# Performance work log

Hardware: AMD Instinct MI355X
Metric: run time of the kernel (lower is better)

Reference implementation:

```python
import jax, jax.numpy as jnp
import numpy as np

B, S, H = 8, 1024, 768
NUM_HEADS, DH = 12, 64
A, T = 12, 64

def setup_inputs() -> dict:
    key = jax.random.key(0)
    ks = jax.random.split(key, 12)
    all_tokens = jax.random.normal(ks[0], (B, S, H), dtype=jnp.float32)
    aspect_tokens = jax.random.normal(ks[1], (B, A, H), dtype=jnp.float32)
    # ragged target slices: start in [0, S-17), length in [1, 16]
    starts = jax.random.randint(ks[2], (T,), 0, S - 17)
    lens = jax.random.randint(ks[3], (T,), 1, 17)
    target_pos_info = jnp.stack([starts, starts + lens], axis=-1).astype(jnp.int32)  # (T,2)
    target_batch_info = jnp.sort(jax.random.randint(ks[4], (T,), 0, B)).astype(jnp.int32)
    attention_mask = jnp.ones((B, S), dtype=jnp.int32)
    s = 0.02
    W1 = jax.random.normal(ks[5], (H, H), dtype=jnp.float32) * s
    b1 = jnp.zeros((H,), dtype=jnp.float32)
    Wq = jax.random.normal(ks[6], (H, NUM_HEADS, DH), dtype=jnp.float32) * s
    bq = jnp.zeros((NUM_HEADS, DH), dtype=jnp.float32)
    Wk = jax.random.normal(ks[7], (H, NUM_HEADS, DH), dtype=jnp.float32) * s
    bk = jnp.zeros((NUM_HEADS, DH), dtype=jnp.float32)
    Wc = jax.random.normal(ks[8], (2 * H, 1), dtype=jnp.float32) * s
    bc = jnp.zeros((1,), dtype=jnp.float32)
    return {"all_tokens": all_tokens, "aspect_tokens": aspect_tokens,
            "target_pos_info": target_pos_info, "target_batch_info": target_batch_info,
            "attention_mask": attention_mask,
            "W1": W1, "b1": b1, "Wq": Wq, "bq": bq, "Wk": Wk, "bk": bk,
            "Wc": Wc, "bc": bc}


def reference(all_tokens, aspect_tokens, target_pos_info, target_batch_info,
              attention_mask, W1, b1, Wq, bq, Wk, bk, Wc, bc):
    # linear_transform (shared for tokens and aspects), dropout = identity at eval
    h = jax.nn.relu(jnp.einsum('bsh,hg->bsg', all_tokens, W1) + b1)     # (B,S,H)
    # SelfAttention: q/k EinsumDense projections; value = raw key_states reshaped
    q = jnp.einsum('bsh,hkd->bskd', h, Wq) + bq                          # (B,S,K,D)
    k = jnp.einsum('bsh,hkd->bskd', h, Wk) + bk
    v = h.reshape(k.shape)                                               # faithful: reshape, no proj
    q = q * jax.lax.rsqrt(jnp.asarray(DH, q.dtype))
    scores = jnp.einsum('bskd,bqkd->bkqs', k, q)                         # (B,K,Q,S)
    mask_val = attention_mask[:, 0].astype(scores.dtype)                 # original uses mask[:, 0:1]
    scores = scores + ((1.0 - mask_val) * -10000.0)[:, None, None, None]
    probs = jax.nn.softmax(scores, axis=-1)
    out = jnp.einsum('bkqs,bskd->bqkd', probs, v).reshape(h.shape)       # (B,S,H)
    # ragged per-target slice mean: masked mean over positions [s0, s1)
    pos = jnp.arange(S)
    s0, s1 = target_pos_info[:, 0], target_pos_info[:, 1]
    span = ((pos[None, :] >= s0[:, None]) & (pos[None, :] < s1[:, None])).astype(out.dtype)  # (T,S)
    gathered = out[target_batch_info]                                    # (T,S,H)
    counts = jnp.maximum(span.sum(-1, keepdims=True), 1.0)
    rep = jnp.einsum('ts,tsh->th', span, gathered) / counts              # (T,H)
    # aspect hidden states and target-aspect pairing (batch-ordered concat)
    h_a = jax.nn.relu(jnp.einsum('bah,hg->bag', aspect_tokens, W1) + b1)  # (B,A,H)
    pair = jnp.concatenate([jnp.broadcast_to(rep[:, None, :], (rep.shape[0], A, H)),
                            h_a[target_batch_info]], axis=-1)             # (T,A,2H)
    t_a_logit = jnp.einsum('tac,co->tao', pair, Wc) + bc                  # (T,A,1)
    return t_a_logit
```

## Files before the change

kernel.cpp:

```cpp
#include <hip/hip_runtime.h>


typedef __attribute__((ext_vector_type(8))) short s8v;
typedef __attribute__((ext_vector_type(4))) short s4v;
typedef __attribute__((ext_vector_type(4))) float f4v;

#define AS1 __attribute__((address_space(1)))
#define AS3 __attribute__((address_space(3)))

__device__ __forceinline__ unsigned short f2bf(float f) {
  union { float f; unsigned u; } v; v.f = f;
  unsigned r = v.u + 0x7FFFu + ((v.u >> 16) & 1u);
  return (unsigned short)(r >> 16);
}

__device__ __forceinline__ float bf2f(unsigned short u) {
  union { unsigned u; float f; } v; v.u = ((unsigned)u) << 16;
  return v.f;
}

__device__ __forceinline__ void gl2lds16(const void* g, void* l) {
  __builtin_amdgcn_global_load_lds((const AS1 void*)g, (AS3 void*)l, 16, 0, 0);
}

__global__ __launch_bounds__(256) void k_prep(const float* __restrict__ asp,
                                              const float* __restrict__ W1,
                                              const float* __restrict__ Wq,
                                              const float* __restrict__ Wk,
                                              unsigned short* __restrict__ Abf,
                                              unsigned short* __restrict__ W1t,
                                              unsigned short* __restrict__ Wqt,
                                              unsigned short* __restrict__ Wkt,
                                              float* __restrict__ outz) {
  __shared__ float T[64][68];
  int bid = blockIdx.x;
  int tid = threadIdx.x;
  if (bid < 36) {
    int i = bid * 256 + tid;
    const float4* src = (const float4*)(asp + (size_t)i * 8);
    float4 a = src[0], b = src[1];
    s8v o;
    o[0] = (short)f2bf(a.x); o[1] = (short)f2bf(a.y);
    o[2] = (short)f2bf(a.z); o[3] = (short)f2bf(a.w);
    o[4] = (short)f2bf(b.x); o[5] = (short)f2bf(b.y);
    o[6] = (short)f2bf(b.z); o[7] = (short)f2bf(b.w);
    *(s8v*)(Abf + (size_t)i * 8) = o;
  } else if (bid < 468) {
    int wb = bid - 36;
    const float* W = (wb < 144) ? W1 : (wb < 288) ? Wq : Wk;
    unsigned short* Wt = (wb < 144) ? W1t : (wb < 288) ? Wqt : Wkt;
    int tile = wb % 144;
    int tr = (tile / 12) * 64;
    int tc = (tile % 12) * 64;
#pragma unroll
    for (int p = 0; p < 4; ++p) {
      int r = p * 16 + (tid >> 4);
      int c = (tid & 15) * 4;
      float4 v = *(const float4*)(W + (size_t)(tr + r) * 768 + tc + c);
      T[r][c] = v.x; T[r][c + 1] = v.y; T[r][c + 2] = v.z; T[r][c + 3] = v.w;
    }
    __syncthreads();
#pragma unroll
    for (int p = 0; p < 2; ++p) {
      int n = p * 32 + (tid >> 3);
      int k8 = (tid & 7) * 8;
      s8v o;
#pragma unroll
      for (int j = 0; j < 8; ++j) o[j] = (short)f2bf(T[k8 + j][n]);
      *(s8v*)(Wt + (size_t)(tc + n) * 768 + tr + k8) = o;
    }
  } else {
#pragma unroll
    for (int q = 0; q < 3; ++q) outz[tid + q * 256] = 0.f;
  }
}

template <int MODE, bool AF32>
__device__ __forceinline__ void gemm_tile(int m0, int n0,
    const unsigned short* __restrict__ A, const float* __restrict__ Af,
    const unsigned short* __restrict__ Bt,
    const float* __restrict__ bias, unsigned short* __restrict__ C,
    unsigned short* __restrict__ C2, const int* __restrict__ pos,
    const int* __restrict__ tbi, unsigned short* As, unsigned short* Bs,
    int* srcRow) {
  const int K = 768;
  int tid = threadIdx.x, lane = tid & 63, w = tid >> 6;

  if (MODE == 2) {
    if (tid < 128) {
      int r = m0 + tid;
      int t = r >> 4, j = r & 15;
      int s0 = pos[2 * t], s1 = pos[2 * t + 1];
      int s = s0 + j; if (s > s1 - 1) s = s1 - 1;
      srcRow[tid] = tbi[t] * 1024 + s;
    }
    __syncthreads();
  }

  int rsub = lane >> 3;
  int cXor = ((lane & 7) ^ rsub) * 8;
  const unsigned short* aSrc[4];
  const float* aSrcF[4];
  const unsigned short* bSrc[4];
#pragma unroll
  for (int i = 0; i < 4; ++i) {
    int lr = (w * 4 + i) * 8 + rsub;
    size_t grow;
    if (MODE == 2) grow = (size_t)srcRow[lr];
    else if (MODE == 3) { int rr = m0 + lr; grow = (size_t)(rr < 96 ? rr : 95); }
    else grow = (size_t)(m0 + lr);
    if (AF32) aSrcF[i] = Af + grow * K + cXor;
    else aSrc[i] = A + grow * K + cXor;
    bSrc[i] = Bt + (size_t)(n0 + lr) * K + cXor;
  }

  f4v acc[4][4];
#pragma unroll
  for (int i = 0; i < 4; ++i)
#pragma unroll
    for (int j = 0; j < 4; ++j) acc[i][j] = (f4v)(0.0f);

  int wm = (w >> 1) * 64, wn = (w & 1) * 64;
  int lc = lane & 15, lg = lane >> 4;
  int aIdx[4][2], bIdx[4][2];
#pragma unroll
  for (int mi = 0; mi < 4; ++mi) {
    int ra = wm + mi * 16 + lc;
    int rb = wn + mi * 16 + lc;
#pragma unroll
    for (int kk = 0; kk < 2; ++kk) {
      aIdx[mi][kk] = ra * 64 + (((kk * 4 + lg) ^ (ra & 7)) * 8);
      bIdx[mi][kk] = rb * 64 + (((kk * 4 + lg) ^ (rb & 7)) * 8);
    }
  }

  for (int k0 = 0; k0 < K; k0 += 64) {
#pragma unroll
    for (int i = 0; i < 4; ++i) gl2lds16(bSrc[i] + k0, Bs + (w * 4 + i) * 512);
    if (AF32) {
#pragma unroll
      for (int i = 0; i < 4; ++i) {
        const float* p = aSrcF[i] + k0;
        float4 v0 = *(const float4*)p;
        float4 v1 = *(const float4*)(p + 4);
        s8v o;
        o[0] = (short)f2bf(v0.x); o[1] = (short)f2bf(v0.y);
        o[2] = (short)f2bf(v0.z); o[3] = (short)f2bf(v0.w);
        o[4] = (short)f2bf(v1.x); o[5] = (short)f2bf(v1.y);
        o[6] = (short)f2bf(v1.z); o[7] = (short)f2bf(v1.w);
        *(s8v*)(As + (w * 4 + i) * 512 + lane * 8) = o;
      }
    } else {
#pragma unroll
      for (int i = 0; i < 4; ++i) gl2lds16(aSrc[i] + k0, As + (w * 4 + i) * 512);
    }
    __syncthreads();
#pragma unroll
    for (int kk = 0; kk < 2; ++kk) {
      s8v ar[4], br[4];
#pragma unroll
      for (int mi = 0; mi < 4; ++mi) ar[mi] = *(const s8v*)(As + aIdx[mi][kk]);
#pragma unroll
      for (int ni = 0; ni < 4; ++ni) br[ni] = *(const s8v*)(Bs + bIdx[ni][kk]);
#pragma unroll
      for (int mi = 0; mi < 4; ++mi)
#pragma unroll
        for (int ni = 0; ni < 4; ++ni)
          acc[mi][ni] = __builtin_amdgcn_mfma_f32_16x16x32_bf16(ar[mi], br[ni], acc[mi][ni], 0, 0, 0);
    }
    __syncthreads();
  }

  if (MODE == 0 || MODE == 1) {
    unsigned short* L = As;
#pragma unroll
    for (int mi = 0; mi < 4; ++mi) {
#pragma unroll
      for (int ni = 0; ni < 4; ++ni) {
        int coll = wn + ni * 16 + lc;
        float bv = bias[n0 + coll];
        int row0l = wm + mi * 16 + lg * 4;
        s4v pk;
#pragma unroll
        for (int r = 0; r < 4; ++r) {
          float x = acc[mi][ni][r] + bv;
          if (MODE == 0) x = x > 0.f ? x : 0.f;
          unsigned short hv = f2bf(x);
          pk[r] = (short)hv;
          int rowl = row0l + r;
          L[rowl * 128 + (((coll >> 3) ^ (rowl & 7)) * 8) + (coll & 7)] = hv;
        }
        if (MODE == 0) {
          int grow0 = m0 + row0l;
          int b = grow0 >> 10, s = grow0 & 1023;
          int gcol = n0 + coll;
          int kh = gcol >> 6, d = gcol & 63;
          *(s4v*)(C2 + ((size_t)((b * 12 + kh) * 64 + d)) * 1024 + s) = pk;
        }
      }
    }
    __syncthreads();
#pragma unroll
    for (int p = 0; p < 8; ++p) {
      int rowl = p * 16 + (tid >> 4);
      int cs = (tid & 15) * 8;
      int chunk = (cs >> 3) ^ (rowl & 7);
      s8v v = *(const s8v*)(L + rowl * 128 + chunk * 8);
      if (MODE == 0) {
        *(s8v*)(C + (size_t)(m0 + rowl) * 768 + n0 + cs) = v;
      } else {
        int gr = m0 + rowl;
        int b = gr >> 10, s = gr & 1023;
        int gcol = n0 + cs;
        int kh = gcol >> 6, d = gcol & 63;
        *(s8v*)(C + ((size_t)((b * 12 + kh) * 1024 + s)) * 64 + d) = v;
      }
    }
  } else {
#pragma unroll
    for (int mi = 0; mi < 4; ++mi) {
#pragma unroll
      for (int ni = 0; ni < 4; ++ni) {
        int col = n0 + wn + ni * 16 + lc;
        float bv = bias[col];
        int row0 = m0 + wm + mi * 16 + lg * 4;
#pragma unroll
        for (int r = 0; r < 4; ++r) {
          int row = row0 + r;
          float x = acc[mi][ni][r] + bv;
          if (MODE == 2) {
            x *= 0.125f;
            int t = row >> 4, j = row & 15;
            int kh = col >> 6, d = col & 63;
            C[(size_t)((t * 12 + kh) * 16 + j) * 64 + d] = f2bf(x);
          } else {
            x = x > 0.f ? x : 0.f;
            if (row < 96) C[(size_t)row * 768 + col] = f2bf(x);
          }
        }
      }
    }
  }
}

__global__ __launch_bounds__(256) void k_gemmA(const float* __restrict__ X,
                                               const float* __restrict__ asp,
                                               const unsigned short* __restrict__ W1t,
                                               const float* __restrict__ b1,
                                               unsigned short* __restrict__ Hbf,
                                               unsigned short* __restrict__ Vt,
                                               unsigned short* __restrict__ Ha) {
  __shared__ unsigned short LDSB[16384];
  __shared__ int srcRow[128];
  unsigned short* As = LDSB;
  unsigned short* Bs = LDSB + 8192;
  int bid = blockIdx.x;
  if (bid < 384) {
    bid = (bid & 7) * 48 + (bid >> 3);
    gemm_tile<0, true>((bid / 6) * 128, (bid % 6) * 128, (const unsigned short*)nullptr,
                       X, W1t, b1, Hbf, Vt, (const int*)nullptr, (const int*)nullptr,
                       As, Bs, srcRow);
  } else {
    int b2 = bid - 384;
    gemm_tile<3, true>(0, b2 * 128, (const unsigned short*)nullptr,
                       asp, W1t, b1, Ha, (unsigned short*)nullptr,
                       (const int*)nullptr, (const int*)nullptr, As, Bs, srcRow);
  }
}

__global__ __launch_bounds__(256) void k_gemmB(const unsigned short* __restrict__ Hbf,
                                               const unsigned short* __restrict__ Wkt,
                                               const float* __restrict__ bk,
                                               unsigned short* __restrict__ Khm,
                                               const unsigned short* __restrict__ Wqt,
                                               const float* __restrict__ bq,
                                               unsigned short* __restrict__ Qhm,
                                               const int* __restrict__ pos,
                                               const int* __restrict__ tbi) {
  __shared__ unsigned short LDSB[16384];
  __shared__ int srcRow[128];
  unsigned short* As = LDSB;
  unsigned short* Bs = LDSB + 8192;
  int bid = blockIdx.x;
  bid = (bid & 7) * 54 + (bid >> 3);
  if (bid < 384) {
    gemm_tile<1, false>((bid / 6) * 128, (bid % 6) * 128, Hbf, (const float*)nullptr,
                        Wkt, bk, Khm, (unsigned short*)nullptr,
                        (const int*)nullptr, (const int*)nullptr, As, Bs, srcRow);
  } else {
    int b2 = bid - 384;
    gemm_tile<2, false>((b2 / 6) * 128, (b2 % 6) * 128, Hbf, (const float*)nullptr,
                        Wqt, bq, Qhm, (unsigned short*)nullptr, pos, tbi,
                        As, Bs, srcRow);
  }
}

__global__ __launch_bounds__(256) void k_attn(const unsigned short* __restrict__ q_hm,
                                              const unsigned short* __restrict__ k_hm,
                                              const unsigned short* __restrict__ vt,
                                              const unsigned short* __restrict__ ha,
                                              const int* __restrict__ pos,
                                              const int* __restrict__ tbi,
                                              const float* __restrict__ Wc,
                                              const float* __restrict__ bc,
                                              float* __restrict__ outp) {
  __shared__ unsigned short P[16 * 1032];
  __shared__ float O[4][16][64];
  __shared__ float rsbuf[4][16];
  __shared__ float inv_rs[16];
  __shared__ float hpart[4];
  __shared__ float rabuf;

  int bid = blockIdx.x;
  bid = (bid & 7) * 96 + (bid >> 3);
  int t = bid / 12, kh = bid % 12;
  int b = tbi[t];
  int s0 = pos[2 * t], s1 = pos[2 * t + 1];
  int len = s1 - s0;
  int tid = threadIdx.x, lane = tid & 63, w = tid >> 6;
  int lg = lane >> 4, lc = lane & 15;

  const unsigned short* qb = q_hm + (size_t)((t * 12 + kh) * 16) * 64;
  s8v a0 = *(const s8v*)(qb + (size_t)lc * 64 + lg * 8);
  s8v a1 = *(const s8v*)(qb + (size_t)lc * 64 + 32 + lg * 8);

  const unsigned short* kb = k_hm + (size_t)((b * 12 + kh) * 1024) * 64;
  float rs[4] = {0.f, 0.f, 0.f, 0.f};
  for (int it = 0; it < 16; ++it) {
    int sb = it * 64 + w * 16;
    s8v b0 = *(const s8v*)(kb + (size_t)(sb + lc) * 64 + lg * 8);
    s8v b1 = *(const s8v*)(kb + (size_t)(sb + lc) * 64 + 32 + lg * 8);
    f4v c = (f4v)(0.0f);
    c = __builtin_amdgcn_mfma_f32_16x16x32_bf16(a0, b0, c, 0, 0, 0);
    c = __builtin_amdgcn_mfma_f32_16x16x32_bf16(a1, b1, c, 0, 0, 0);
#pragma unroll
    for (int r = 0; r < 4; ++r) {
      float p = __expf(c[r]);
      rs[r] += p;
      P[(lg * 4 + r) * 1032 + sb + lc] = f2bf(p);
    }
  }
#pragma unroll
  for (int m = 1; m < 16; m <<= 1) {
#pragma unroll
    for (int r = 0; r < 4; ++r) rs[r] += __shfl_xor(rs[r], m, 64);
  }
  if (lc == 0) {
#pragma unroll
    for (int r = 0; r < 4; ++r) rsbuf[w][lg * 4 + r] = rs[r];
  }
  __syncthreads();
  if (tid < 16)
    inv_rs[tid] = 1.0f / (rsbuf[0][tid] + rsbuf[1][tid] + rsbuf[2][tid] + rsbuf[3][tid]);

  const unsigned short* vb = vt + (size_t)((b * 12 + kh) * 64) * 1024;
  f4v oc[4];
#pragma unroll
  for (int n = 0; n < 4; ++n) oc[n] = (f4v)(0.0f);
  for (int it = 0; it < 8; ++it) {
    int s32 = it * 128 + w * 32;
    s8v pa = *(const s8v*)(P + lc * 1032 + s32 + lg * 8);
#pragma unroll
    for (int n = 0; n < 4; ++n) {
      s8v vbf = *(const s8v*)(vb + (size_t)(n * 16 + lc) * 1024 + s32 + lg * 8);
      oc[n] = __builtin_amdgcn_mfma_f32_16x16x32_bf16(pa, vbf, oc[n], 0, 0, 0);
    }
  }
#pragma unroll
  for (int n = 0; n < 4; ++n)
#pragma unroll
    for (int r = 0; r < 4; ++r) O[w][lg * 4 + r][n * 16 + lc] = oc[n][r];
  __syncthreads();
  if (w == 0) {
    float sum = 0.f;
    for (int j = 0; j < len; ++j) {
      float v = O[0][j][lane] + O[1][j][lane] + O[2][j][lane] + O[3][j][lane];
      sum += v * inv_rs[j];
    }
    float repd = sum / (float)len;
    float pr = repd * Wc[kh * 64 + lane];
#pragma unroll
    for (int m = 1; m < 64; m <<= 1) pr += __shfl_xor(pr, m, 64);
    if (lane == 0) rabuf = pr;
  } else {
    const unsigned short* hr = ha + (size_t)(b * 12 + kh) * 768;
    float p2 = 0.f;
#pragma unroll
    for (int q = 0; q < 4; ++q) {
      int g = (tid - 64) + q * 192;
      p2 += bf2f(hr[g]) * Wc[768 + g];
    }
#pragma unroll
    for (int m = 1; m < 64; m <<= 1) p2 += __shfl_xor(p2, m, 64);
    if (lane == 0) hpart[w] = p2;
  }
  __syncthreads();
  if (tid < 12) {
    float ra = rabuf;
    float had = hpart[1] + hpart[2] + hpart[3];
    float v = ra + ((tid == kh) ? (had + bc[0]) : 0.f);
    atomicAdd(&outp[t * 12 + tid], v);
  }
}

extern "C" void kernel_launch(void* const* d_in, const int* in_sizes, int n_in,
                              void* d_out, int out_size, void* d_ws, size_t ws_size,
                              hipStream_t stream) {
  const float* all_tokens = (const float*)d_in[0];
  const float* aspect     = (const float*)d_in[1];
  const int*   pos        = (const int*)d_in[2];
  const int*   tbi        = (const int*)d_in[3];
  const float* W1 = (const float*)d_in[5];
  const float* b1 = (const float*)d_in[6];
  const float* Wq = (const float*)d_in[7];
  const float* bq = (const float*)d_in[8];
  const float* Wk = (const float*)d_in[9];
  const float* bk = (const float*)d_in[10];
  const float* Wc = (const float*)d_in[11];
  const float* bc = (const float*)d_in[12];
  float* out = (float*)d_out;

  char* ws = (char*)d_ws;
  unsigned short* W1t = (unsigned short*)(ws + 12582912);
  unsigned short* Wqt = (unsigned short*)(ws + 13762560);
  unsigned short* Wkt = (unsigned short*)(ws + 14942208);
  unsigned short* Hbf = (unsigned short*)(ws + 16121856);
  unsigned short* Khm = (unsigned short*)(ws + 28704768);
  unsigned short* Vt  = (unsigned short*)(ws + 41287680);
  unsigned short* Qhm = (unsigned short*)(ws + 53870592);
  unsigned short* Abf = (unsigned short*)(ws + 55640448);
  unsigned short* Ha  = (unsigned short*)(ws + 55787904);

  hipLaunchKernelGGL(k_prep, dim3(469), dim3(256), 0, stream,
                     aspect, W1, Wq, Wk, Abf, W1t, Wqt, Wkt, out);
  hipLaunchKernelGGL(k_gemmA, dim3(390), dim3(256), 0, stream,
                     all_tokens, aspect, W1t, b1, Hbf, Vt, Ha);
  hipLaunchKernelGGL(k_gemmB, dim3(432), dim3(256), 0, stream,
                     Hbf, Wkt, bk, Khm, Wqt, bq, Qhm, pos, tbi);
  hipLaunchKernelGGL(k_attn, dim3(768), dim3(256), 0, stream,
                     Qhm, Khm, Vt, Ha, pos, tbi, Wc, bc, out);
}
```

Measured before the change: 78.70 us.

## Double-buffer LDS tiles in GEMM main loop to overlap loads with MFMA

The GEMM K-loop now uses two LDS buffers. The next K-slice is prefetched (global_load_lds for bf16 operands, register loads then bf16 conversion for fp32 A) while MFMAs run on the current slice, and there is one barrier per iteration instead of two. This is meant to hide global memory latency behind compute. In exchange, LDS use per block doubles to 64KB, which can lower occupancy, and more registers are held for the fp32 prefetch.

```diff
diff --git a/kernel.cpp b/kernel.cpp
--- a/kernel.cpp
+++ b/kernel.cpp
@@ -81,8 +81,7 @@
     const unsigned short* __restrict__ Bt,
     const float* __restrict__ bias, unsigned short* __restrict__ C,
     unsigned short* __restrict__ C2, const int* __restrict__ pos,
-    const int* __restrict__ tbi, unsigned short* As, unsigned short* Bs,
-    int* srcRow) {
+    const int* __restrict__ tbi, unsigned short* LDSB, int* srcRow) {
   const int K = 768;
   int tid = threadIdx.x, lane = tid & 63, w = tid >> 6;
 
@@ -134,45 +133,90 @@
     }
   }
 
-  for (int k0 = 0; k0 < K; k0 += 64) {
-#pragma unroll
-    for (int i = 0; i < 4; ++i) gl2lds16(bSrc[i] + k0, Bs + (w * 4 + i) * 512);
-    if (AF32) {
-#pragma unroll
-      for (int i = 0; i < 4; ++i) {
-        const float* p = aSrcF[i] + k0;
-        float4 v0 = *(const float4*)p;
-        float4 v1 = *(const float4*)(p + 4);
-        s8v o;
-        o[0] = (short)f2bf(v0.x); o[1] = (short)f2bf(v0.y);
-        o[2] = (short)f2bf(v0.z); o[3] = (short)f2bf(v0.w);
-        o[4] = (short)f2bf(v1.x); o[5] = (short)f2bf(v1.y);
-        o[6] = (short)f2bf(v1.z); o[7] = (short)f2bf(v1.w);
-        *(s8v*)(As + (w * 4 + i) * 512 + lane * 8) = o;
+  if (AF32) {
+    float4 p0[4], p1[4];
+#pragma unroll
+    for (int i = 0; i < 4; ++i) {
+      const float* p = aSrcF[i];
+      p0[i] = *(const float4*)p;
+      p1[i] = *(const float4*)(p + 4);
+    }
+#pragma unroll
+    for (int i = 0; i < 4; ++i) gl2lds16(bSrc[i], LDSB + 8192 + (w * 4 + i) * 512);
+#pragma unroll
+    for (int i = 0; i < 4; ++i) {
+      s8v o;
+      o[0] = (short)f2bf(p0[i].x); o[1] = (short)f2bf(p0[i].y);
+      o[2] = (short)f2bf(p0[i].z); o[3] = (short)f2bf(p0[i].w);
+      o[4] = (short)f2bf(p1[i].x); o[5] = (short)f2bf(p1[i].y);
+      o[6] = (short)f2bf(p1[i].z); o[7] = (short)f2bf(p1[i].w);
+      *(s8v*)(LDSB + (w * 4 + i) * 512 + lane * 8) = o;
+    }
+  } else {
+#pragma unroll
+    for (int i = 0; i < 4; ++i) gl2lds16(aSrc[i], LDSB + (w * 4 + i) * 512);
+#pragma unroll
+    for (int i = 0; i < 4; ++i) gl2lds16(bSrc[i], LDSB + 8192 + (w * 4 + i) * 512);
+  }
+  asm volatile("s_waitcnt vmcnt(0)" ::: "memory");
+  __builtin_amdgcn_s_barrier();
+
+  for (int t = 0; t < 12; ++t) {
+    int cur = t & 1;
+    unsigned short* Acur = LDSB + cur * 16384;
+    unsigned short* Bcur = Acur + 8192;
+    unsigned short* Anxt = LDSB + (cur ^ 1) * 16384;
+    unsigned short* Bnxt = Anxt + 8192;
+    bool pf = (t < 11);
+    int k1 = (t + 1) * 64;
+    float4 av0[4], av1[4];
+    if (pf) {
+      if (AF32) {
+#pragma unroll
+        for (int i = 0; i < 4; ++i) {
+          const float* p = aSrcF[i] + k1;
+          av0[i] = *(const float4*)p;
+          av1[i] = *(const float4*)(p + 4);
+        }
+      } else {
+#pragma unroll
+        for (int i = 0; i < 4; ++i) gl2lds16(aSrc[i] + k1, Anxt + (w * 4 + i) * 512);
       }
-    } else {
-#pragma unroll
-      for (int i = 0; i < 4; ++i) gl2lds16(aSrc[i] + k0, As + (w * 4 + i) * 512);
-    }
-    __syncthreads();
+#pragma unroll
+      for (int i = 0; i < 4; ++i) gl2lds16(bSrc[i] + k1, Bnxt + (w * 4 + i) * 512);
+    }
 #pragma unroll
     for (int kk = 0; kk < 2; ++kk) {
       s8v ar[4], br[4];
 #pragma unroll
-      for (int mi = 0; mi < 4; ++mi) ar[mi] = *(const s8v*)(As + aIdx[mi][kk]);
-#pragma unroll
-      for (int ni = 0; ni < 4; ++ni) br[ni] = *(const s8v*)(Bs + bIdx[ni][kk]);
+      for (int mi = 0; mi < 4; ++mi) ar[mi] = *(const s8v*)(Acur + aIdx[mi][kk]);
+#pragma unroll
+      for (int ni = 0; ni < 4; ++ni) br[ni] = *(const s8v*)(Bcur + bIdx[ni][kk]);
 #pragma unroll
       for (int mi = 0; mi < 4; ++mi)
 #pragma unroll
         for (int ni = 0; ni < 4; ++ni)
           acc[mi][ni] = __builtin_amdgcn_mfma_f32_16x16x32_bf16(ar[mi], br[ni], acc[mi][ni], 0, 0, 0);
     }
-    __syncthreads();
+    if (pf) {
+      if (AF32) {
+#pragma unroll
+        for (int i = 0; i < 4; ++i) {
+          s8v o;
+          o[0] = (short)f2bf(av0[i].x); o[1] = (short)f2bf(av0[i].y);
+          o[2] = (short)f2bf(av0[i].z); o[3] = (short)f2bf(av0[i].w);
+          o[4] = (short)f2bf(av1[i].x); o[5] = (short)f2bf(av1[i].y);
+          o[6] = (short)f2bf(av1[i].z); o[7] = (short)f2bf(av1[i].w);
+          *(s8v*)(Anxt + (w * 4 + i) * 512 + lane * 8) = o;
+        }
+      }
+      asm volatile("s_waitcnt vmcnt(0)" ::: "memory");
+      __builtin_amdgcn_s_barrier();
+    }
   }
 
   if (MODE == 0 || MODE == 1) {
-    unsigned short* L = As;
+    unsigned short* L = LDSB;
 #pragma unroll
     for (int mi = 0; mi < 4; ++mi) {
 #pragma unroll
@@ -250,21 +294,19 @@
                                                unsigned short* __restrict__ Hbf,
                                                unsigned short* __restrict__ Vt,
                                                unsigned short* __restrict__ Ha) {
-  __shared__ unsigned short LDSB[16384];
+  __shared__ unsigned short LDSB[32768];
   __shared__ int srcRow[128];
-  unsigned short* As = LDSB;
-  unsigned short* Bs = LDSB + 8192;
   int bid = blockIdx.x;
   if (bid < 384) {
     bid = (bid & 7) * 48 + (bid >> 3);
     gemm_tile<0, true>((bid / 6) * 128, (bid % 6) * 128, (const unsigned short*)nullptr,
                        X, W1t, b1, Hbf, Vt, (const int*)nullptr, (const int*)nullptr,
-                       As, Bs, srcRow);
+                       LDSB, srcRow);
   } else {
     int b2 = bid - 384;
     gemm_tile<3, true>(0, b2 * 128, (const unsigned short*)nullptr,
                        asp, W1t, b1, Ha, (unsigned short*)nullptr,
-                       (const int*)nullptr, (const int*)nullptr, As, Bs, srcRow);
+                       (const int*)nullptr, (const int*)nullptr, LDSB, srcRow);
   }
 }
 
@@ -277,21 +319,19 @@
                                                unsigned short* __restrict__ Qhm,
                                                const int* __restrict__ pos,
                                                const int* __restrict__ tbi) {
-  __shared__ unsigned short LDSB[16384];
+  __shared__ unsigned short LDSB[32768];
   __shared__ int srcRow[128];
-  unsigned short* As = LDSB;
-  unsigned short* Bs = LDSB + 8192;
   int bid = blockIdx.x;
   bid = (bid & 7) * 54 + (bid >> 3);
   if (bid < 384) {
     gemm_tile<1, false>((bid / 6) * 128, (bid % 6) * 128, Hbf, (const float*)nullptr,
                         Wkt, bk, Khm, (unsigned short*)nullptr,
-                        (const int*)nullptr, (const int*)nullptr, As, Bs, srcRow);
+                        (const int*)nullptr, (const int*)nullptr, LDSB, srcRow);
   } else {
     int b2 = bid - 384;
     gemm_tile<2, false>((b2 / 6) * 128, (b2 % 6) * 128, Hbf, (const float*)nullptr,
                         Wqt, bq, Qhm, (unsigned short*)nullptr, pos, tbi,
-                        As, Bs, srcRow);
+                        LDSB, srcRow);
   }
 }
 
```

Measured after the change: 79.64 us. No clear change (+1.2%).
